# Kernel optimization log

Hardware: AMD Instinct MI355X
Metric: run time of the kernel (lower is better)

## Reference

```python
import jax, jax.numpy as jnp
import numpy as np

B, N, EMB, H, C = 1, 4096, 256, 4, 64  # heads*C == 256 feeds Linear(256, EMB)
NEG_SLOPE = 0.2
LN_EPS = 1e-5


def setup_inputs() -> dict:
    key = jax.random.key(0)
    ks = jax.random.split(key, 8)
    x = jax.random.normal(ks[0], (B, N, EMB), jnp.float32)
    adj = jax.random.randint(ks[1], (B, N, N), 0, 2, jnp.int32)
    W_lin = jax.random.normal(ks[2], (EMB, H * C), jnp.float32) * (1.0 / EMB) ** 0.5
    att_src = jax.random.normal(ks[3], (H, C), jnp.float32) * 0.1
    att_dst = jax.random.normal(ks[4], (H, C), jnp.float32) * 0.1
    bias_att = jax.random.normal(ks[5], (H * C,), jnp.float32) * 0.02
    W_out = jax.random.normal(ks[6], (H * C, EMB), jnp.float32) * (1.0 / (H * C)) ** 0.5
    b_out = jax.random.normal(ks[7], (EMB,), jnp.float32) * 0.02
    gamma = jnp.ones((EMB,), jnp.float32)
    beta = jnp.zeros((EMB,), jnp.float32)
    return dict(x=x, adj=adj, W_lin=W_lin, att_src=att_src, att_dst=att_dst,
                bias_att=bias_att, W_out=W_out, b_out=b_out, gamma=gamma, beta=beta)


def reference(x, adj, W_lin, att_src, att_dst, bias_att, W_out, b_out, gamma, beta):
    # DenseGATConv (concat=True, add_loop=True, negative_slope=0.2)
    h = (x @ W_lin).reshape(B, N, H, C)                       # [B,N,H,C]
    a_src = jnp.einsum('bnhc,hc->bnh', h, att_src)            # per source node j
    a_dst = jnp.einsum('bnhc,hc->bnh', h, att_dst)            # per dest node i
    # alpha[b,i,j,h] = a_src[b,j,h] + a_dst[b,i,h]
    alpha = a_src[:, None, :, :] + a_dst[:, :, None, :]       # [B,N,N,H]
    alpha = jnp.where(alpha >= 0, alpha, NEG_SLOPE * alpha)   # leaky_relu
    # add self-loops to adjacency, then mask and softmax over source axis j
    idx = jnp.arange(N)
    adj_sl = adj.at[:, idx, idx].set(1)
    alpha = jnp.where(adj_sl[..., None] == 0, -jnp.inf, alpha)
    alpha = jax.nn.softmax(alpha, axis=2)                     # [B,N,N,H]
    out = jnp.einsum('bijh,bjhc->bihc', alpha, h)             # aggregate sources
    out = out.reshape(B, N, H * C) + bias_att                 # concat heads + GAT bias
    # trailing Linear + LayerNorm
    y = out @ W_out + b_out                                   # [B,N,EMB]
    mu = jnp.mean(y, axis=-1, keepdims=True)
    var = jnp.mean((y - mu) ** 2, axis=-1, keepdims=True)
    return (y - mu) * jax.lax.rsqrt(var + LN_EPS) * gamma + beta
```

## Files before the change

kernel.cpp:

```cpp
#include <hip/hip_runtime.h>
#include <stdint.h>

#define N    4096
#define EMB  256
#define NH   4
#define HC   64
#define PAD  40

typedef __attribute__((ext_vector_type(8))) short s16x8;
typedef __attribute__((ext_vector_type(4))) short s16x4;
typedef __attribute__((ext_vector_type(4))) float f32x4;
typedef __attribute__((ext_vector_type(4))) int   i32x4;
typedef unsigned short ushort_t;

__device__ __forceinline__ unsigned short f2bf(float f) {
  unsigned int u = __builtin_bit_cast(unsigned int, f);
  u += 0x7fffu + ((u >> 16) & 1u);
  return (unsigned short)(u >> 16);
}

__global__ __launch_bounds__(256)
void k_prep(const float* __restrict__ W0, ushort_t* __restrict__ WP0,
            const float* __restrict__ W1, ushort_t* __restrict__ WP1,
            const int* __restrict__ adj, unsigned int* __restrict__ abits)
{
  int b = blockIdx.x;
  if (b < 4096) {
    const int i = b;
    const int t = threadIdx.x;
    const int* src = adj + (size_t)i * N + t * 16;
    i32x4 v0 = *(const i32x4*)(src);
    i32x4 v1 = *(const i32x4*)(src + 4);
    i32x4 v2 = *(const i32x4*)(src + 8);
    i32x4 v3 = *(const i32x4*)(src + 12);
    unsigned int m = 0;
    #pragma unroll
    for (int u = 0; u < 4; ++u) {
      m |= (v0[u] != 0 ? 1u : 0u) << u;
      m |= (v1[u] != 0 ? 1u : 0u) << (4 + u);
      m |= (v2[u] != 0 ? 1u : 0u) << (8 + u);
      m |= (v3[u] != 0 ? 1u : 0u) << (12 + u);
    }
    if ((i >> 4) == t) m |= 1u << (i & 15);
    unsigned int partner = __shfl_xor(m, 1);
    if ((t & 1) == 0) {
      unsigned int word = m | (partner << 16);
      abits[(size_t)(t >> 1) * N + i] = word;
    }
  } else {
    b -= 4096;
    int k = b & 255;
    int m = threadIdx.x;
    size_t dst = ((size_t)(k >> 5) * 256 + m) * 32 + (k & 31);
    if (b < 256) WP0[dst] = f2bf(W0[k * EMB + m]);
    else         WP1[dst] = f2bf(W1[k * EMB + m]);
  }
}

__global__ __launch_bounds__(256, 2)
void k1_gemm_h(const float* __restrict__ x,
               const ushort_t* __restrict__ WlP,
               const float* __restrict__ att_src,
               const float* __restrict__ att_dst,
               ushort_t* __restrict__ hS,
               float* __restrict__ a_srcT,
               float* __restrict__ a_dstT)
{
  __shared__ ushort_t T_lds[64][PAD];
  __shared__ float red_lds[2][2][32];
  const int t = threadIdx.x;
  const int lane = t & 63;
  const int w = t >> 6;
  const int ihalf = w & 1, chalf = w >> 1;
  const int i0 = blockIdx.x * 32;
  const int head = blockIdx.y;
  const int c0 = head * 64;
  const int lq = lane >> 4, lm = lane & 15;

  f32x4 acc[2];
  acc[0] = f32x4{0.f, 0.f, 0.f, 0.f};
  acc[1] = f32x4{0.f, 0.f, 0.f, 0.f};

  const float* xrow = x + (size_t)(i0 + ihalf * 16 + lm) * EMB + lq * 8;
  const ushort_t* wp0 = WlP + (size_t)(c0 + chalf * 32 + lm) * 32 + lq * 8;
  const ushort_t* wp1 = WlP + (size_t)(c0 + chalf * 32 + 16 + lm) * 32 + lq * 8;

  #pragma unroll 2
  for (int kp = 0; kp < 8; ++kp) {
    f32x4 v0 = *(const f32x4*)(xrow + kp * 32);
    f32x4 v1 = *(const f32x4*)(xrow + kp * 32 + 4);
    s16x8 a;
    a[0]=(short)f2bf(v0[0]); a[1]=(short)f2bf(v0[1]); a[2]=(short)f2bf(v0[2]); a[3]=(short)f2bf(v0[3]);
    a[4]=(short)f2bf(v1[0]); a[5]=(short)f2bf(v1[1]); a[6]=(short)f2bf(v1[2]); a[7]=(short)f2bf(v1[3]);
    s16x8 b0 = *(const s16x8*)(wp0 + (size_t)kp * 8192);
    s16x8 b1 = *(const s16x8*)(wp1 + (size_t)kp * 8192);
    acc[0] = __builtin_amdgcn_mfma_f32_16x16x32_bf16(a, b0, acc[0], 0, 0, 0);
    acc[1] = __builtin_amdgcn_mfma_f32_16x16x32_bf16(a, b1, acc[1], 0, 0, 0);
  }

  float ps[4] = {0.f,0.f,0.f,0.f}, pd[4] = {0.f,0.f,0.f,0.f};
  #pragma unroll
  for (int nf = 0; nf < 2; ++nf) {
    int c = chalf * 32 + nf * 16 + lm;
    float wsv = att_src[c0 + c];
    float wdv = att_dst[c0 + c];
    #pragma unroll
    for (int r = 0; r < 4; ++r) {
      float v = acc[nf][r];
      T_lds[c][ihalf * 16 + lq * 4 + r] = f2bf(v);
      ps[r] += v * wsv;
      pd[r] += v * wdv;
    }
  }
  #pragma unroll
  for (int r = 0; r < 4; ++r) {
    #pragma unroll
    for (int mm = 1; mm < 16; mm <<= 1) {
      ps[r] += __shfl_xor(ps[r], mm);
      pd[r] += __shfl_xor(pd[r], mm);
    }
  }
  if (lm == 0) {
    #pragma unroll
    for (int r = 0; r < 4; ++r) {
      int node = ihalf * 16 + lq * 4 + r;
      red_lds[0][chalf][node] = ps[r];
      red_lds[1][chalf][node] = pd[r];
    }
  }
  __syncthreads();
  if (t < 32) {
    a_srcT[head * N + i0 + t] = red_lds[0][0][t] + red_lds[0][1][t];
    a_dstT[head * N + i0 + t] = red_lds[1][0][t] + red_lds[1][1][t];
  }
  {
    int c = t >> 2, seg = t & 3;
    s16x8 v = *(const s16x8*)&T_lds[c][seg * 8];
    size_t base = (((size_t)head * 128 + (i0 >> 5)) * 64 + c) * 32 + seg * 8;
    *(s16x8*)(hS + base) = v;
  }
}

__global__ __launch_bounds__(512, 2)
void k34_attn(const unsigned int* __restrict__ abits,
              const ushort_t* __restrict__ hS,
              const float* __restrict__ a_srcT,
              const float* __restrict__ a_dstT,
              const float* __restrict__ bias_att,
              ushort_t* __restrict__ oS)
{
  __shared__ float acc_lds[7][32][65];
  __shared__ float l_lds[8][32];

  const int t = threadIdx.x;
  const int lane = t & 63;
  const int jq = t >> 6;
  const int head = blockIdx.y;
  const int i0 = blockIdx.x * 32;
  const int lm = lane & 15, lq = lane >> 4;
  const int ig0 = i0 + lm;
  const int ig1 = i0 + 16 + lm;

  const float* asrc_h = a_srcT + head * N;
  const ushort_t* hS_h = hS + (size_t)head * 128 * 64 * 32;
  const float ad0 = a_dstT[head * N + ig0];
  const float ad1 = a_dstT[head * N + ig1];

  f32x4 acc[2][4];
  #pragma unroll
  for (int s = 0; s < 2; ++s)
    #pragma unroll
    for (int nf = 0; nf < 4; ++nf) acc[s][nf] = f32x4{0.f, 0.f, 0.f, 0.f};
  float lp0 = 0.f, lp1 = 0.f;

  #pragma unroll 2
  for (int it = 0; it < 16; ++it) {
    const int jw = jq * 16 + it;
    const int jl = jw * 32 + lq * 8;

    unsigned int word0 = abits[(size_t)jw * N + ig0];
    unsigned int word1 = abits[(size_t)jw * N + ig1];
    f32x4 as0 = *(const f32x4*)(asrc_h + jl);
    f32x4 as1 = *(const f32x4*)(asrc_h + jl + 4);

    const ushort_t* tile = hS_h + (size_t)jw * 2048;
    s16x8 b0 = *(const s16x8*)(tile + ( 0 + lm) * 32 + lq * 8);
    s16x8 b1 = *(const s16x8*)(tile + (16 + lm) * 32 + lq * 8);
    s16x8 b2 = *(const s16x8*)(tile + (32 + lm) * 32 + lq * 8);
    s16x8 b3 = *(const s16x8*)(tile + (48 + lm) * 32 + lq * 8);

    unsigned int e0[8], e1[8];
    #pragma unroll
    for (int jj = 0; jj < 8; ++jj) {
      float asv = (jj < 4) ? as0[jj] : as1[jj - 4];
      float sc0 = asv + ad0;
      float sc1 = asv + ad1;
      sc0 = fmaxf(sc0, 0.2f * sc0);
      sc1 = fmaxf(sc1, 0.2f * sc1);
      bool c0 = (word0 >> (lq * 8 + jj)) & 1u;
      bool c1 = (word1 >> (lq * 8 + jj)) & 1u;
      float v0 = c0 ? __expf(sc0) : 0.f;
      float v1 = c1 ? __expf(sc1) : 0.f;
      unsigned int eb0 = __builtin_bit_cast(unsigned int, v0) & 0xffff0000u;
      unsigned int eb1 = __builtin_bit_cast(unsigned int, v1) & 0xffff0000u;
      e0[jj] = eb0;
      e1[jj] = eb1;
      lp0 += __builtin_bit_cast(float, eb0);
      lp1 += __builtin_bit_cast(float, eb1);
    }
    i32x4 p0, p1;
    #pragma unroll
    for (int u = 0; u < 4; ++u) {
      p0[u] = (int)__builtin_amdgcn_perm(e0[2 * u + 1], e0[2 * u], 0x07060302u);
      p1[u] = (int)__builtin_amdgcn_perm(e1[2 * u + 1], e1[2 * u], 0x07060302u);
    }
    s16x8 af0 = __builtin_bit_cast(s16x8, p0);
    s16x8 af1 = __builtin_bit_cast(s16x8, p1);

    acc[0][0] = __builtin_amdgcn_mfma_f32_16x16x32_bf16(af0, b0, acc[0][0], 0, 0, 0);
    acc[0][1] = __builtin_amdgcn_mfma_f32_16x16x32_bf16(af0, b1, acc[0][1], 0, 0, 0);
    acc[0][2] = __builtin_amdgcn_mfma_f32_16x16x32_bf16(af0, b2, acc[0][2], 0, 0, 0);
    acc[0][3] = __builtin_amdgcn_mfma_f32_16x16x32_bf16(af0, b3, acc[0][3], 0, 0, 0);
    acc[1][0] = __builtin_amdgcn_mfma_f32_16x16x32_bf16(af1, b0, acc[1][0], 0, 0, 0);
    acc[1][1] = __builtin_amdgcn_mfma_f32_16x16x32_bf16(af1, b1, acc[1][1], 0, 0, 0);
    acc[1][2] = __builtin_amdgcn_mfma_f32_16x16x32_bf16(af1, b2, acc[1][2], 0, 0, 0);
    acc[1][3] = __builtin_amdgcn_mfma_f32_16x16x32_bf16(af1, b3, acc[1][3], 0, 0, 0);
  }

  lp0 += __shfl_xor(lp0, 16);
  lp0 += __shfl_xor(lp0, 32);
  lp1 += __shfl_xor(lp1, 16);
  lp1 += __shfl_xor(lp1, 32);
  if (lq == 0) {
    l_lds[jq][lm] = lp0;
    l_lds[jq][16 + lm] = lp1;
  }

  if (jq != 0) {
    #pragma unroll
    for (int s = 0; s < 2; ++s)
      #pragma unroll
      for (int nf = 0; nf < 4; ++nf)
        #pragma unroll
        for (int r = 0; r < 4; ++r)
          acc_lds[jq - 1][s * 16 + lq * 4 + r][nf * 16 + lm] = acc[s][nf][r];
  }
  __syncthreads();
  if (jq == 0) {
    #pragma unroll
    for (int s = 0; s < 2; ++s) {
      float linv[4];
      #pragma unroll
      for (int r = 0; r < 4; ++r) {
        int row = s * 16 + lq * 4 + r;
        float sum = 0.f;
        #pragma unroll
        for (int q = 0; q < 8; ++q) sum += l_lds[q][row];
        linv[r] = 1.f / sum;
      }
      #pragma unroll
      for (int nf = 0; nf < 4; ++nf) {
        float bia = bias_att[head * 64 + nf * 16 + lm];
        #pragma unroll
        for (int r = 0; r < 4; ++r) {
          int row = s * 16 + lq * 4 + r;
          float v = acc[s][nf][r];
          #pragma unroll
          for (int q = 0; q < 7; ++q) v += acc_lds[q][row][nf * 16 + lm];
          size_t idx = (((size_t)((i0 >> 4) + s) * 8) + head * 2 + (nf >> 1)) * 512
                     + (lq * 4 + r) * 32 + (nf & 1) * 16 + lm;
          oS[idx] = f2bf(v * linv[r] + bia);
        }
      }
    }
  }
}

__global__ __launch_bounds__(256, 2)
void k5_gemm_ln(const ushort_t* __restrict__ oS,
                const ushort_t* __restrict__ WoP,
                const float* __restrict__ b_out,
                const float* __restrict__ gamma,
                const float* __restrict__ beta,
                float* __restrict__ out)
{
  __shared__ float y_lds[16][260];
  const int t = threadIdx.x, lane = t & 63, w = t >> 6;
  const int i0 = blockIdx.x * 16;
  const int lq = lane >> 4, lm = lane & 15;

  f32x4 acc[4];
  #pragma unroll
  for (int nf = 0; nf < 4; ++nf) acc[nf] = f32x4{0.f, 0.f, 0.f, 0.f};

  const ushort_t* oS_b = oS + (size_t)(i0 >> 4) * 4096 + lm * 32 + lq * 8;
  const ushort_t* wp0 = WoP + (size_t)(w * 64 +  0 + lm) * 32 + lq * 8;
  const ushort_t* wp1 = WoP + (size_t)(w * 64 + 16 + lm) * 32 + lq * 8;
  const ushort_t* wp2 = WoP + (size_t)(w * 64 + 32 + lm) * 32 + lq * 8;
  const ushort_t* wp3 = WoP + (size_t)(w * 64 + 48 + lm) * 32 + lq * 8;

  #pragma unroll 2
  for (int kp = 0; kp < 8; ++kp) {
    s16x8 a  = *(const s16x8*)(oS_b + (size_t)kp * 512);
    s16x8 b0 = *(const s16x8*)(wp0 + (size_t)kp * 8192);
    s16x8 b1 = *(const s16x8*)(wp1 + (size_t)kp * 8192);
    s16x8 b2 = *(const s16x8*)(wp2 + (size_t)kp * 8192);
    s16x8 b3 = *(const s16x8*)(wp3 + (size_t)kp * 8192);
    acc[0] = __builtin_amdgcn_mfma_f32_16x16x32_bf16(a, b0, acc[0], 0, 0, 0);
    acc[1] = __builtin_amdgcn_mfma_f32_16x16x32_bf16(a, b1, acc[1], 0, 0, 0);
    acc[2] = __builtin_amdgcn_mfma_f32_16x16x32_bf16(a, b2, acc[2], 0, 0, 0);
    acc[3] = __builtin_amdgcn_mfma_f32_16x16x32_bf16(a, b3, acc[3], 0, 0, 0);
  }
  #pragma unroll
  for (int nf = 0; nf < 4; ++nf)
    #pragma unroll
    for (int r = 0; r < 4; ++r) {
      int row = lq * 4 + r;
      int col = w * 64 + nf * 16 + lm;
      y_lds[row][col] = acc[nf][r] + b_out[col];
    }
  __syncthreads();
  f32x4 g  = *(const f32x4*)(gamma + lane * 4);
  f32x4 be = *(const f32x4*)(beta + lane * 4);
  #pragma unroll
  for (int r = w * 4; r < w * 4 + 4; ++r) {
    f32x4 v = *(const f32x4*)&y_lds[r][lane * 4];
    float s1 = v[0] + v[1] + v[2] + v[3];
    float s2 = v[0]*v[0] + v[1]*v[1] + v[2]*v[2] + v[3]*v[3];
    #pragma unroll
    for (int mm = 1; mm < 64; mm <<= 1) { s1 += __shfl_xor(s1, mm); s2 += __shfl_xor(s2, mm); }
    float mu = s1 * (1.f / 256.f);
    float var = s2 * (1.f / 256.f) - mu * mu;
    float rs = rsqrtf(var + 1e-5f);
    f32x4 o;
    #pragma unroll
    for (int u = 0; u < 4; ++u) o[u] = (v[u] - mu) * rs * g[u] + be[u];
    *(f32x4*)(out + (size_t)(i0 + r) * EMB + lane * 4) = o;
  }
}

extern "C" void kernel_launch(void* const* d_in, const int* in_sizes, int n_in,
                              void* d_out, int out_size, void* d_ws, size_t ws_size,
                              hipStream_t stream)
{
  (void)in_sizes; (void)n_in; (void)out_size; (void)ws_size;
  const float* x        = (const float*)d_in[0];
  const int*   adj      = (const int*)d_in[1];
  const float* W_lin    = (const float*)d_in[2];
  const float* att_src  = (const float*)d_in[3];
  const float* att_dst  = (const float*)d_in[4];
  const float* bias_att = (const float*)d_in[5];
  const float* W_out    = (const float*)d_in[6];
  const float* b_out    = (const float*)d_in[7];
  const float* gamma    = (const float*)d_in[8];
  const float* beta     = (const float*)d_in[9];
  float* out = (float*)d_out;

  uint8_t* p = (uint8_t*)d_ws;
  ushort_t* WlP = (ushort_t*)p;  p += (size_t)EMB * EMB * sizeof(ushort_t);
  ushort_t* WoP = (ushort_t*)p;  p += (size_t)EMB * EMB * sizeof(ushort_t);
  ushort_t* hS  = (ushort_t*)p;  p += (size_t)NH * HC * N * sizeof(ushort_t);
  float* a_srcb = (float*)p;     p += (size_t)NH * N * sizeof(float);
  float* a_dstb = (float*)p;     p += (size_t)NH * N * sizeof(float);
  ushort_t* oS  = (ushort_t*)p;  p += (size_t)N * EMB * sizeof(ushort_t);
  unsigned int* abits = (unsigned int*)p; p += (size_t)(N / 32) * N * sizeof(unsigned int);

  k_prep<<<4096 + 512, 256, 0, stream>>>(W_lin, WlP, W_out, WoP, adj, abits);
  k1_gemm_h<<<dim3(N / 32, NH), 256, 0, stream>>>(x, WlP, att_src, att_dst, hS, a_srcb, a_dstb);
  k34_attn<<<dim3(N / 32, NH), 512, 0, stream>>>(abits, hS, a_srcb, a_dstb, bias_att, oS);
  k5_gemm_ln<<<N / 16, 256, 0, stream>>>(oS, WoP, b_out, gamma, beta, out);
}
```

Measured before the change: 165.6 us.

## Double attention destination tile to 64 rows and use exp2 with prescaled logits

The attention kernel now handles 64 destination rows per block instead of 32. Each loaded hS B-fragment and a_src vector is reused across four MFMA row groups, and the grid shrinks to 256 blocks. The cross-wave reduction runs in two passes so the existing LDS buffer can be reused. Logits are prescaled by log2(e) in the projection kernel so the inner loop can call the hardware exp2 directly. The cost is higher register pressure: launch bounds drop to 1 block per CU, and 256 blocks means lower occupancy and fewer waves to hide latency.

After: 166.3 us (median of 2 runs). About the same (+0.4%).

```diff
diff --git a/kernel.cpp b/kernel.cpp
--- a/kernel.cpp
+++ b/kernel.cpp
@@ -6,6 +6,7 @@
 #define NH   4
 #define HC   64
 #define PAD  40
+#define LOG2E 1.4426950408889634f
 
 typedef __attribute__((ext_vector_type(8))) short s16x8;
 typedef __attribute__((ext_vector_type(4))) short s16x4;
@@ -130,8 +131,8 @@
   }
   __syncthreads();
   if (t < 32) {
-    a_srcT[head * N + i0 + t] = red_lds[0][0][t] + red_lds[0][1][t];
-    a_dstT[head * N + i0 + t] = red_lds[1][0][t] + red_lds[1][1][t];
+    a_srcT[head * N + i0 + t] = (red_lds[0][0][t] + red_lds[0][1][t]) * LOG2E;
+    a_dstT[head * N + i0 + t] = (red_lds[1][0][t] + red_lds[1][1][t]) * LOG2E;
   }
   {
     int c = t >> 2, seg = t & 3;
@@ -141,7 +142,7 @@
   }
 }
 
-__global__ __launch_bounds__(512, 2)
+__global__ __launch_bounds__(512, 1)
 void k34_attn(const unsigned int* __restrict__ abits,
               const ushort_t* __restrict__ hS,
               const float* __restrict__ a_srcT,
@@ -150,36 +151,37 @@
               ushort_t* __restrict__ oS)
 {
   __shared__ float acc_lds[7][32][65];
-  __shared__ float l_lds[8][32];
+  __shared__ float l_lds[8][64];
 
   const int t = threadIdx.x;
   const int lane = t & 63;
   const int jq = t >> 6;
   const int head = blockIdx.y;
-  const int i0 = blockIdx.x * 32;
+  const int i0 = blockIdx.x * 64;
   const int lm = lane & 15, lq = lane >> 4;
-  const int ig0 = i0 + lm;
-  const int ig1 = i0 + 16 + lm;
 
   const float* asrc_h = a_srcT + head * N;
   const ushort_t* hS_h = hS + (size_t)head * 128 * 64 * 32;
-  const float ad0 = a_dstT[head * N + ig0];
-  const float ad1 = a_dstT[head * N + ig1];
-
-  f32x4 acc[2][4];
-  #pragma unroll
-  for (int s = 0; s < 2; ++s)
+  float ad[4];
+  #pragma unroll
+  for (int s = 0; s < 4; ++s) ad[s] = a_dstT[head * N + i0 + s * 16 + lm];
+
+  f32x4 acc[4][4];
+  #pragma unroll
+  for (int s = 0; s < 4; ++s)
     #pragma unroll
     for (int nf = 0; nf < 4; ++nf) acc[s][nf] = f32x4{0.f, 0.f, 0.f, 0.f};
-  float lp0 = 0.f, lp1 = 0.f;
+  float lp[4] = {0.f, 0.f, 0.f, 0.f};
 
   #pragma unroll 2
   for (int it = 0; it < 16; ++it) {
     const int jw = jq * 16 + it;
     const int jl = jw * 32 + lq * 8;
 
-    unsigned int word0 = abits[(size_t)jw * N + ig0];
-    unsigned int word1 = abits[(size_t)jw * N + ig1];
+    unsigned int word[4];
+    #pragma unroll
+    for (int s = 0; s < 4; ++s)
+      word[s] = abits[(size_t)jw * N + i0 + s * 16 + lm];
     f32x4 as0 = *(const f32x4*)(asrc_h + jl);
     f32x4 as1 = *(const f32x4*)(asrc_h + jl + 4);
 
@@ -189,87 +191,81 @@
     s16x8 b2 = *(const s16x8*)(tile + (32 + lm) * 32 + lq * 8);
     s16x8 b3 = *(const s16x8*)(tile + (48 + lm) * 32 + lq * 8);
 
-    unsigned int e0[8], e1[8];
-    #pragma unroll
-    for (int jj = 0; jj < 8; ++jj) {
-      float asv = (jj < 4) ? as0[jj] : as1[jj - 4];
-      float sc0 = asv + ad0;
-      float sc1 = asv + ad1;
-      sc0 = fmaxf(sc0, 0.2f * sc0);
-      sc1 = fmaxf(sc1, 0.2f * sc1);
-      bool c0 = (word0 >> (lq * 8 + jj)) & 1u;
-      bool c1 = (word1 >> (lq * 8 + jj)) & 1u;
-      float v0 = c0 ? __expf(sc0) : 0.f;
-      float v1 = c1 ? __expf(sc1) : 0.f;
-      unsigned int eb0 = __builtin_bit_cast(unsigned int, v0) & 0xffff0000u;
-      unsigned int eb1 = __builtin_bit_cast(unsigned int, v1) & 0xffff0000u;
-      e0[jj] = eb0;
-      e1[jj] = eb1;
-      lp0 += __builtin_bit_cast(float, eb0);
-      lp1 += __builtin_bit_cast(float, eb1);
-    }
-    i32x4 p0, p1;
-    #pragma unroll
-    for (int u = 0; u < 4; ++u) {
-      p0[u] = (int)__builtin_amdgcn_perm(e0[2 * u + 1], e0[2 * u], 0x07060302u);
-      p1[u] = (int)__builtin_amdgcn_perm(e1[2 * u + 1], e1[2 * u], 0x07060302u);
-    }
-    s16x8 af0 = __builtin_bit_cast(s16x8, p0);
-    s16x8 af1 = __builtin_bit_cast(s16x8, p1);
-
-    acc[0][0] = __builtin_amdgcn_mfma_f32_16x16x32_bf16(af0, b0, acc[0][0], 0, 0, 0);
-    acc[0][1] = __builtin_amdgcn_mfma_f32_16x16x32_bf16(af0, b1, acc[0][1], 0, 0, 0);
-    acc[0][2] = __builtin_amdgcn_mfma_f32_16x16x32_bf16(af0, b2, acc[0][2], 0, 0, 0);
-    acc[0][3] = __builtin_amdgcn_mfma_f32_16x16x32_bf16(af0, b3, acc[0][3], 0, 0, 0);
-    acc[1][0] = __builtin_amdgcn_mfma_f32_16x16x32_bf16(af1, b0, acc[1][0], 0, 0, 0);
-    acc[1][1] = __builtin_amdgcn_mfma_f32_16x16x32_bf16(af1, b1, acc[1][1], 0, 0, 0);
-    acc[1][2] = __builtin_amdgcn_mfma_f32_16x16x32_bf16(af1, b2, acc[1][2], 0, 0, 0);
-    acc[1][3] = __builtin_amdgcn_mfma_f32_16x16x32_bf16(af1, b3, acc[1][3], 0, 0, 0);
-  }
-
-  lp0 += __shfl_xor(lp0, 16);
-  lp0 += __shfl_xor(lp0, 32);
-  lp1 += __shfl_xor(lp1, 16);
-  lp1 += __shfl_xor(lp1, 32);
+    #pragma unroll
+    for (int s = 0; s < 4; ++s) {
+      unsigned int e[8];
+      #pragma unroll
+      for (int jj = 0; jj < 8; ++jj) {
+        float asv = (jj < 4) ? as0[jj] : as1[jj - 4];
+        float sc = asv + ad[s];
+        sc = fmaxf(sc, 0.2f * sc);
+        bool con = (word[s] >> (lq * 8 + jj)) & 1u;
+        float v = con ? __builtin_amdgcn_exp2f(sc) : 0.f;
+        unsigned int eb = __builtin_bit_cast(unsigned int, v) & 0xffff0000u;
+        e[jj] = eb;
+        lp[s] += __builtin_bit_cast(float, eb);
+      }
+      i32x4 pk;
+      #pragma unroll
+      for (int u = 0; u < 4; ++u)
+        pk[u] = (int)__builtin_amdgcn_perm(e[2 * u + 1], e[2 * u], 0x07060302u);
+      s16x8 af = __builtin_bit_cast(s16x8, pk);
+      acc[s][0] = __builtin_amdgcn_mfma_f32_16x16x32_bf16(af, b0, acc[s][0], 0, 0, 0);
+      acc[s][1] = __builtin_amdgcn_mfma_f32_16x16x32_bf16(af, b1, acc[s][1], 0, 0, 0);
+      acc[s][2] = __builtin_amdgcn_mfma_f32_16x16x32_bf16(af, b2, acc[s][2], 0, 0, 0);
+      acc[s][3] = __builtin_amdgcn_mfma_f32_16x16x32_bf16(af, b3, acc[s][3], 0, 0, 0);
+    }
+  }
+
+  #pragma unroll
+  for (int s = 0; s < 4; ++s) {
+    lp[s] += __shfl_xor(lp[s], 16);
+    lp[s] += __shfl_xor(lp[s], 32);
+  }
   if (lq == 0) {
-    l_lds[jq][lm] = lp0;
-    l_lds[jq][16 + lm] = lp1;
-  }
-
-  if (jq != 0) {
-    #pragma unroll
-    for (int s = 0; s < 2; ++s)
+    #pragma unroll
+    for (int s = 0; s < 4; ++s) l_lds[jq][s * 16 + lm] = lp[s];
+  }
+
+  #pragma unroll
+  for (int pass = 0; pass < 2; ++pass) {
+    __syncthreads();
+    if (jq != 0) {
       #pragma unroll
-      for (int nf = 0; nf < 4; ++nf)
+      for (int s = 0; s < 2; ++s)
         #pragma unroll
-        for (int r = 0; r < 4; ++r)
-          acc_lds[jq - 1][s * 16 + lq * 4 + r][nf * 16 + lm] = acc[s][nf][r];
-  }
-  __syncthreads();
-  if (jq == 0) {
-    #pragma unroll
-    for (int s = 0; s < 2; ++s) {
-      float linv[4];
+        for (int nf = 0; nf < 4; ++nf)
+          #pragma unroll
+          for (int r = 0; r < 4; ++r)
+            acc_lds[jq - 1][s * 16 + lq * 4 + r][nf * 16 + lm] = acc[pass * 2 + s][nf][r];
+    }
+    __syncthreads();
+    if (jq == 0) {
       #pragma unroll
-      for (int r = 0; r < 4; ++r) {
-        int row = s * 16 + lq * 4 + r;
-        float sum = 0.f;
-        #pragma unroll
-        for (int q = 0; q < 8; ++q) sum += l_lds[q][row];
-        linv[r] = 1.f / sum;
-      }
-      #pragma unroll
-      for (int nf = 0; nf < 4; ++nf) {
-        float bia = bias_att[head * 64 + nf * 16 + lm];
+      for (int s = 0; s < 2; ++s) {
+        const int sg = pass * 2 + s;
+        float linv[4];
         #pragma unroll
         for (int r = 0; r < 4; ++r) {
-          int row = s * 16 + lq * 4 + r;
-          float v = acc[s][nf][r];
+          int row = sg * 16 + lq * 4 + r;
+          float sum = 0.f;
           #pragma unroll
-          for (int q = 0; q < 7; ++q) v += acc_lds[q][row][nf * 16 + lm];
-          size_t idx = (((size_t)((i0 >> 4) + s) * 8) + head * 2 + (nf >> 1)) * 512
-                     + (lq * 4 + r) * 32 + (nf & 1) * 16 + lm;
-          oS[idx] = f2bf(v * linv[r] + bia);
+          for (int q = 0; q < 8; ++q) sum += l_lds[q][row];
+          linv[r] = 1.f / sum;
+        }
+        #pragma unroll
+        for (int nf = 0; nf < 4; ++nf) {
+          float bia = bias_att[head * 64 + nf * 16 + lm];
+          #pragma unroll
+          for (int r = 0; r < 4; ++r) {
+            float v = acc[sg][nf][r];
+            #pragma unroll
+            for (int q = 0; q < 7; ++q)
+              v += acc_lds[q][s * 16 + lq * 4 + r][nf * 16 + lm];
+            size_t idx = (((size_t)((i0 >> 4) + sg) * 8) + head * 2 + (nf >> 1)) * 512
+                       + (lq * 4 + r) * 32 + (nf & 1) * 16 + lm;
+            oS[idx] = f2bf(v * linv[r] + bia);
+          }
         }
       }
     }
@@ -367,6 +363,6 @@
 
   k_prep<<<4096 + 512, 256, 0, stream>>>(W_lin, WlP, W_out, WoP, adj, abits);
   k1_gemm_h<<<dim3(N / 32, NH), 256, 0, stream>>>(x, WlP, att_src, att_dst, hS, a_srcb, a_dstb);
-  k34_attn<<<dim3(N / 32, NH), 512, 0, stream>>>(abits, hS, a_srcb, a_dstb, bias_att, oS);
+  k34_attn<<<dim3(N / 64, NH), 512, 0, stream>>>(abits, hS, a_srcb, a_dstb, bias_att, oS);
   k5_gemm_ln<<<N / 16, 256, 0, stream>>>(oS, WoP, b_out, gamma, beta, out);
 }
```
